# Kernel tuning notes

Hardware: AMD Instinct MI355X
Metric: run time of the kernel (lower is better)

The kernel has to match this reference:

```python
import jax, jax.numpy as jnp
import numpy as np
import math
from itertools import combinations

SEQ_LEN = 8
SET_SIZE = 3
IN_DIM = 2048
OUT_DIM = 1152
WAY = 5
SHOT = 5
N_QUERIES = 200
PE_SCALE = 0.1
LN_EPS = 1e-5
NEG_INF = -1e30

TUPLES = np.array(list(combinations(range(SEQ_LEN), SET_SIZE)), dtype=np.int32)  # [56, 3]
TUPLES_LEN = TUPLES.shape[0]


def _positional_encoding(d_model, max_len):
    position = np.arange(max_len)[:, None].astype(np.float32)
    div_term = np.exp(np.arange(0, d_model, 2).astype(np.float32) * -(math.log(10000.0) / d_model))
    pe = np.zeros((max_len, d_model), dtype=np.float32)
    pe[:, 0::2] = np.sin(position * div_term) * PE_SCALE
    pe[:, 1::2] = np.cos(position * div_term) * PE_SCALE
    return jnp.asarray(pe)

PE = _positional_encoding(IN_DIM, int(SEQ_LEN * 1.5))


def setup_inputs() -> dict:
    key = jax.random.key(0)
    ks = jax.random.split(key, 6)
    support_set = jax.random.normal(ks[0], (WAY * SHOT, SEQ_LEN, IN_DIM), dtype=jnp.float32)
    queries = jax.random.normal(ks[1], (N_QUERIES, SEQ_LEN, IN_DIM), dtype=jnp.float32)
    support_labels = jnp.repeat(jnp.arange(WAY, dtype=jnp.int32), SHOT)  # [25]
    Wk = jax.random.normal(ks[2], (IN_DIM * SET_SIZE, OUT_DIM), dtype=jnp.float32) * 0.02
    bk = jnp.zeros((OUT_DIM,), dtype=jnp.float32)
    Wv = jax.random.normal(ks[3], (IN_DIM * SET_SIZE, OUT_DIM), dtype=jnp.float32) * 0.02
    bv = jnp.zeros((OUT_DIM,), dtype=jnp.float32)
    ln_g = jnp.ones((OUT_DIM,), dtype=jnp.float32)
    ln_b = jnp.zeros((OUT_DIM,), dtype=jnp.float32)
    return {"support_set": support_set, "support_labels": support_labels, "queries": queries,
            "Wk": Wk, "bk": bk, "Wv": Wv, "bv": bv, "ln_g": ln_g, "ln_b": ln_b}


def _layernorm(x, g, b):
    mu = jnp.mean(x, axis=-1, keepdims=True)
    var = jnp.var(x, axis=-1, keepdims=True)
    return (x - mu) * jax.lax.rsqrt(var + LN_EPS) * g + b


def _tuple_features(x):
    # x: [N, SEQ_LEN, IN_DIM]; add PE (dropout is identity at inference), gather frame tuples.
    n = x.shape[0]
    x = x + PE[None, :x.shape[1], :]
    return x[:, TUPLES, :].reshape(n, TUPLES_LEN, SET_SIZE * IN_DIM)  # [N, 56, 6144]


def reference(support_set, support_labels, queries, Wk, bk, Wv, bv, ln_g, ln_b):
    n_q = queries.shape[0]
    s_feat = _tuple_features(support_set)   # [S, T, 6144]
    q_feat = _tuple_features(queries)       # [Q, T, 6144]

    sk = _layernorm(s_feat @ Wk + bk, ln_g, ln_b)  # [S, T, D]
    qk = _layernorm(q_feat @ Wk + bk, ln_g, ln_b)  # [Q, T, D]
    sv = s_feat @ Wv + bv                           # [S, T, D]
    qv = q_feat @ Wv + bv                           # [Q, T, D]

    # scores between every query tuple and every support tuple
    scores = jnp.einsum('qtd,skd->qtsk', qk, sk) / math.sqrt(OUT_DIM)  # [Q, T, S, T]

    # per-class masked softmax over (support clips of class c) x (support tuples)
    class_mask = support_labels[None, :] == jnp.arange(WAY, dtype=support_labels.dtype)[:, None]  # [WAY, S]
    masked = scores[None] + jnp.where(class_mask[:, None, None, :, None], 0.0, NEG_INF)  # [WAY, Q, T, S, T]
    attn = jax.nn.softmax(masked.reshape(WAY, n_q, TUPLES_LEN, -1), axis=-1)
    attn = attn.reshape(WAY, n_q, TUPLES_LEN, -1, TUPLES_LEN)  # [WAY, Q, T, S, T]

    proto = jnp.einsum('cqtsk,skd->cqtd', attn, sv)  # [WAY, Q, T, D]
    diff = qv[None] - proto                           # [WAY, Q, T, D]
    dist = -jnp.sum(diff * diff, axis=(2, 3)) / TUPLES_LEN  # [WAY, Q]
    return dist.T  # logits [Q, WAY]
```

## Files before the change

kernel.cpp:

```cpp
#include <hip/hip_runtime.h>
#include <math.h>

#define SEQ_LEN 8
#define IN_DIM 2048
#define OUT_DIM 1152
#define NTUP 56
#define NSUP 25
#define NQ 200
#define WAY 5
#define SFRAMES 200
#define NFRAMES 1800
#define SROWS 1400
#define QROWS 11200
#define AT_STRIDE 1440
#define KC 288
#define ALD 296

typedef __attribute__((ext_vector_type(8))) short short8;
typedef __attribute__((ext_vector_type(4))) float f32x4;

__device__ __constant__ int TUP[NTUP][3] = {
{0,1,2},{0,1,3},{0,1,4},{0,1,5},{0,1,6},{0,1,7},
{0,2,3},{0,2,4},{0,2,5},{0,2,6},{0,2,7},
{0,3,4},{0,3,5},{0,3,6},{0,3,7},
{0,4,5},{0,4,6},{0,4,7},
{0,5,6},{0,5,7},
{0,6,7},
{1,2,3},{1,2,4},{1,2,5},{1,2,6},{1,2,7},
{1,3,4},{1,3,5},{1,3,6},{1,3,7},
{1,4,5},{1,4,6},{1,4,7},
{1,5,6},{1,5,7},
{1,6,7},
{2,3,4},{2,3,5},{2,3,6},{2,3,7},
{2,4,5},{2,4,6},{2,4,7},
{2,5,6},{2,5,7},
{2,6,7},
{3,4,5},{3,4,6},{3,4,7},
{3,5,6},{3,5,7},
{3,6,7},
{4,5,6},{4,5,7},
{4,6,7},
{5,6,7}};

__device__ __forceinline__ unsigned short f2bf(float x) {
  union { float f; unsigned int u; } v; v.f = x;
  unsigned int r = v.u + 0x7fffu + ((v.u >> 16) & 1u);
  return (unsigned short)(r >> 16);
}
__device__ __forceinline__ float bf2f(unsigned short s) {
  union { float f; unsigned int u; } v; v.u = ((unsigned int)s) << 16;
  return v.f;
}

__device__ __forceinline__ void gll16(const void* g, void* l) {
  __builtin_amdgcn_global_load_lds(
      (const __attribute__((address_space(1))) unsigned int*)g,
      (__attribute__((address_space(3))) unsigned int*)l, 16, 0, 0);
}

#define APB_OFF   0UL
#define WT_OFF    7372800UL
#define PB_OFF    35684352UL
#define QKB_OFF   60567552UL
#define SKB_OFF   86372352UL
#define QVB_OFF   89597952UL
#define SVB_OFF   115402752UL
#define G2_OFF    118628352UL
#define SCB_OFF   119457792UL
#define G1B_OFF   151713792UL
#define QNORM_OFF 183969792UL
#define RANK_OFF  184014592UL

__global__ __launch_bounds__(256) void k_pre(const float* __restrict__ S,
                                             const float* __restrict__ Q,
                                             const float* __restrict__ Wk,
                                             const float* __restrict__ Wv,
                                             const int* __restrict__ labels,
                                             unsigned short* __restrict__ APb,
                                             unsigned short* __restrict__ WT,
                                             int* __restrict__ rank,
                                             float* __restrict__ outz) {
  __shared__ float t[32][33];
  int b = blockIdx.x, tid = threadIdx.x;
  if (b < NFRAMES) {
    int frame = b;
    int e8 = tid * 8;
    int pos = frame & 7;
    const float c0 = -logf(10000.0f) / (float)IN_DIM;
    float pe[8];
#pragma unroll
    for (int p = 0; p < 4; ++p) {
      float dt = expf((float)(e8 + 2 * p) * c0);
      float arg = (float)pos * dt;
      pe[2 * p] = sinf(arg) * 0.1f;
      pe[2 * p + 1] = cosf(arg) * 0.1f;
    }
    const float* src = (frame < SFRAMES) ? (S + (size_t)frame * IN_DIM + e8)
                                         : (Q + (size_t)(frame - SFRAMES) * IN_DIM + e8);
    float4 x0 = ((const float4*)src)[0], x1 = ((const float4*)src)[1];
    short8 o;
    o[0] = (short)f2bf(x0.x + pe[0]); o[1] = (short)f2bf(x0.y + pe[1]);
    o[2] = (short)f2bf(x0.z + pe[2]); o[3] = (short)f2bf(x0.w + pe[3]);
    o[4] = (short)f2bf(x1.x + pe[4]); o[5] = (short)f2bf(x1.y + pe[5]);
    o[6] = (short)f2bf(x1.z + pe[6]); o[7] = (short)f2bf(x1.w + pe[7]);
    *(short8*)(APb + (size_t)frame * IN_DIM + e8) = o;
  } else if (b < NFRAMES + 13824) {
    int z = b - NFRAMES;
    int bz = z / (64 * 36); int rem = z % (64 * 36);
    int by = rem / 64, bx = rem % 64;
    int w = bz / 3, j = bz % 3;
    const float* W = w ? Wv : Wk;
    int k0 = bx * 32, d0 = by * 32;
    int tx = tid & 31, ty = tid >> 5;
#pragma unroll
    for (int i = 0; i < 4; ++i) {
      int k = k0 + ty + i * 8;
      t[ty + i * 8][tx] = W[(size_t)(j * IN_DIM + k) * OUT_DIM + d0 + tx];
    }
    __syncthreads();
    int colbase = w * 3456 + j * 1152 + d0;
#pragma unroll
    for (int i = 0; i < 4; ++i) {
      int d = ty + i * 8;
      WT[(size_t)(colbase + d) * IN_DIM + k0 + tx] = f2bf(t[tx][d]);
    }
  } else {
    for (int i = tid; i < NQ * WAY; i += 256) outz[i] = 0.f;
    if (tid == 0) {
      for (int s = 0; s < NSUP; ++s) {
        int r = 0;
        for (int s2 = 0; s2 < NSUP; ++s2)
          r += (labels[s2] < labels[s]) || (labels[s2] == labels[s] && s2 < s);
        rank[s] = r;
      }
    }
  }
}

__device__ __forceinline__ void mfma_core(const short* __restrict__ A, int lda, int maxA,
                                          const short* __restrict__ B, int ldb, int maxB,
                                          int K, short* lds, f32x4 (&acc)[4][4]) {
  int tid = threadIdx.x;
  int lane = tid & 63, wave = tid >> 6;
  int wm = wave & 1, wn = wave >> 1;
  int col = lane & 15, quad = lane >> 4;
  short* As = lds;
  short* Bs = lds + 4096;
  int s0 = tid, s1 = tid + 256;
  int r0 = s0 >> 2, r1 = s1 >> 2;
  int o0 = (s0 & 3) * 8, o1 = (s1 & 3) * 8;
  const short* a0p = A + (size_t)min(r0, maxA) * lda + o0;
  const short* a1p = A + (size_t)min(r1, maxA) * lda + o1;
  const short* b0p = B + (size_t)min(r0, maxB) * ldb + o0;
  const short* b1p = B + (size_t)min(r1, maxB) * ldb + o1;
  short* la0 = As + s0 * 8; short* la1 = As + s1 * 8;
  short* lb0 = Bs + s0 * 8; short* lb1 = Bs + s1 * 8;

  for (int k0 = 0; k0 < K; k0 += 32) {
    gll16(a0p + k0, la0);
    gll16(a1p + k0, la1);
    gll16(b0p + k0, lb0);
    gll16(b1p + k0, lb1);
    __syncthreads();
    short8 af[4], bf[4];
#pragma unroll
    for (int i = 0; i < 4; ++i)
      af[i] = *(const short8*)(As + (wm * 64 + i * 16 + col) * 32 + quad * 8);
#pragma unroll
    for (int j = 0; j < 4; ++j)
      bf[j] = *(const short8*)(Bs + (wn * 64 + j * 16 + col) * 32 + quad * 8);
#pragma unroll
    for (int i = 0; i < 4; ++i)
#pragma unroll
      for (int j = 0; j < 4; ++j)
        acc[i][j] = __builtin_amdgcn_mfma_f32_16x16x32_bf16(af[i], bf[j], acc[i][j], 0, 0, 0);
    __syncthreads();
  }
}

__global__ __launch_bounds__(256) void k_gemm1(const unsigned short* __restrict__ APb,
                                               const unsigned short* __restrict__ WT,
                                               unsigned short* __restrict__ Pb) {
  __shared__ short lds[8192];
  int row0 = blockIdx.y * 128, col0 = blockIdx.x * 128;
  f32x4 acc[4][4];
#pragma unroll
  for (int i = 0; i < 4; ++i)
#pragma unroll
    for (int j = 0; j < 4; ++j) acc[i][j] = (f32x4)(0.f);
  mfma_core((const short*)APb + (size_t)row0 * IN_DIM, IN_DIM, min(127, NFRAMES - 1 - row0),
            (const short*)WT + (size_t)col0 * IN_DIM, IN_DIM, 127,
            IN_DIM, lds, acc);
  int lane = threadIdx.x & 63, wave = threadIdx.x >> 6;
  int wm = wave & 1, wn = wave >> 1, col = lane & 15, quad = lane >> 4;
#pragma unroll
  for (int i = 0; i < 4; ++i)
#pragma unroll
    for (int r = 0; r < 4; ++r) {
      int gr = row0 + wm * 64 + i * 16 + quad * 4 + r;
      if (gr >= NFRAMES) continue;
#pragma unroll
      for (int j = 0; j < 4; ++j)
        Pb[(size_t)gr * 6912 + col0 + wn * 64 + j * 16 + col] = f2bf(acc[i][j][r]);
    }
}

__global__ __launch_bounds__(256) void k_combine(const unsigned short* __restrict__ Pb,
                                                 const float* __restrict__ bk,
                                                 const float* __restrict__ bv,
                                                 const float* __restrict__ g,
                                                 const float* __restrict__ bb,
                                                 const int* __restrict__ rank,
                                                 unsigned short* __restrict__ SKb,
                                                 unsigned short* __restrict__ QKb,
                                                 unsigned short* __restrict__ SVb,
                                                 unsigned short* __restrict__ QVb,
                                                 float* __restrict__ qnorm) {
  __shared__ short L[8 * 3456];
  int n = blockIdx.x, w = blockIdx.y;
  int tid = threadIdx.x;
  bool sup = n < NSUP;
  int fbase = sup ? n * SEQ_LEN : SFRAMES + (n - NSUP) * SEQ_LEN;
  for (int i = 0; i < 14; ++i) {
    int idx = tid + 256 * i;
    if (idx < 3456) {
      int fr = idx / 432, off = (idx - fr * 432) * 8;
      *(short8*)(L + fr * 3456 + off) =
          *(const short8*)(Pb + (size_t)(fbase + fr) * 6912 + w * 3456 + off);
    }
  }
  __syncthreads();
  int wave = tid >> 6, lane = tid & 63;
  const float* bias = w ? bv : bk;
  float2 bi[9], gg[9], bbv[9];
#pragma unroll
  for (int i = 0; i < 9; ++i) {
    int p = lane + 64 * i;
    bi[i] = *(const float2*)(bias + 2 * p);
    if (w == 0) {
      gg[i] = *(const float2*)(g + 2 * p);
      bbv[i] = *(const float2*)(bb + 2 * p);
    }
  }
  int obase = sup ? rank[n] * NTUP : (n - NSUP) * NTUP;
  const unsigned int* Lu = (const unsigned int*)L;
  for (int t = wave; t < NTUP; t += 4) {
    int b0 = (TUP[t][0] * 3456) >> 1;
    int b1 = (TUP[t][1] * 3456 + 1152) >> 1;
    int b2 = (TUP[t][2] * 3456 + 2304) >> 1;
    float va[18];
    float sum = 0.f, sq = 0.f;
#pragma unroll
    for (int i = 0; i < 9; ++i) {
      int p = lane + 64 * i;
      unsigned int u0 = Lu[b0 + p], u1 = Lu[b1 + p], u2 = Lu[b2 + p];
      float a = bf2f((unsigned short)u0) + bf2f((unsigned short)u1) +
                bf2f((unsigned short)u2) + bi[i].x;
      float b = bf2f((unsigned short)(u0 >> 16)) + bf2f((unsigned short)(u1 >> 16)) +
                bf2f((unsigned short)(u2 >> 16)) + bi[i].y;
      va[2 * i] = a; va[2 * i + 1] = b;
      sum += a + b;
      sq += a * a + b * b;
    }
#pragma unroll
    for (int o = 32; o; o >>= 1) {
      sum += __shfl_xor(sum, o);
      sq += __shfl_xor(sq, o);
    }
    int orow = obase + t;
    if (w == 0) {
      float mean = sum * (1.f / OUT_DIM);
      float var = sq * (1.f / OUT_DIM) - mean * mean;
      float inv = rsqrtf(var + 1e-5f);
      unsigned short* outp = (sup ? SKb : QKb) + (size_t)orow * OUT_DIM;
#pragma unroll
      for (int i = 0; i < 9; ++i) {
        int p = lane + 64 * i;
        unsigned int lo = f2bf((va[2 * i] - mean) * inv * gg[i].x + bbv[i].x);
        unsigned int hi = f2bf((va[2 * i + 1] - mean) * inv * gg[i].y + bbv[i].y);
        *(unsigned int*)(outp + 2 * p) = lo | (hi << 16);
      }
    } else {
      unsigned short* outp = (sup ? SVb : QVb) + (size_t)orow * OUT_DIM;
#pragma unroll
      for (int i = 0; i < 9; ++i) {
        int p = lane + 64 * i;
        unsigned int lo = f2bf(va[2 * i]);
        unsigned int hi = f2bf(va[2 * i + 1]);
        *(unsigned int*)(outp + 2 * p) = lo | (hi << 16);
      }
      if (!sup && lane == 0) qnorm[orow] = sq;
    }
  }
}

__global__ __launch_bounds__(256) void k_rowgemm(const unsigned short* __restrict__ QKb,
                                                 const unsigned short* __restrict__ SKb,
                                                 const unsigned short* __restrict__ QVb,
                                                 const unsigned short* __restrict__ SVb,
                                                 unsigned short* __restrict__ SCb,
                                                 unsigned short* __restrict__ G1b,
                                                 unsigned short* __restrict__ G2) {
  __shared__ short lds[8192];
  int L = blockIdx.x;
  f32x4 acc[4][4];
#pragma unroll
  for (int i = 0; i < 4; ++i)
#pragma unroll
    for (int j = 0; j < 4; ++j) acc[i][j] = (f32x4)(0.f);
  int lane = threadIdx.x & 63, wave = threadIdx.x >> 6;
  int wm = wave & 1, wn = wave >> 1, col = lane & 15, quad = lane >> 4;

  if (L < 1936) {
    int l = L, g1 = 0;
    if (l >= 968) { g1 = 1; l -= 968; }
    int rowSub = l & 7, t = l >> 3;
    int colIdx = t % 11, rowGroup = t / 11;
    int row0 = (rowGroup * 8 + rowSub) << 7;
    int col0 = colIdx << 7;
    const unsigned short* Am = g1 ? QVb : QKb;
    const unsigned short* Bm = g1 ? SVb : SKb;
    mfma_core((const short*)Am + (size_t)row0 * OUT_DIM, OUT_DIM, min(127, QROWS - 1 - row0),
              (const short*)Bm + (size_t)col0 * OUT_DIM, OUT_DIM, min(127, SROWS - 1 - col0),
              OUT_DIM, lds, acc);
    unsigned short* outp = g1 ? G1b : SCb;
    const float scl = g1 ? 1.0f : 0.029462782549439483f;
#pragma unroll
    for (int i = 0; i < 4; ++i)
#pragma unroll
      for (int r = 0; r < 4; ++r) {
        int gr = row0 + wm * 64 + i * 16 + quad * 4 + r;
        if (gr >= QROWS) continue;
#pragma unroll
        for (int j = 0; j < 4; ++j) {
          int gc = col0 + wn * 64 + j * 16 + col;
          if (gc < SROWS) {
            int c = gc / 280;
            outp[(size_t)gr * AT_STRIDE + gc + c * 8] = f2bf(acc[i][j][r] * scl);
          }
        }
      }
  } else {
    int l = L - 1936;
    int c = l / 9, rem = l % 9;
    int i0 = (rem / 3) << 7, j0 = (rem % 3) << 7;
    const short* base = (const short*)SVb + (size_t)c * 280 * OUT_DIM;
    mfma_core(base + (size_t)i0 * OUT_DIM, OUT_DIM, min(127, 279 - i0),
              base + (size_t)j0 * OUT_DIM, OUT_DIM, min(127, 279 - j0),
              OUT_DIM, lds, acc);
    unsigned short* g2c = G2 + (size_t)c * KC * KC;
#pragma unroll
    for (int i = 0; i < 4; ++i)
#pragma unroll
      for (int r = 0; r < 4; ++r) {
        int gi = i0 + wm * 64 + i * 16 + quad * 4 + r;
        if (gi >= KC) continue;
#pragma unroll
        for (int j = 0; j < 4; ++j) {
          int gj = j0 + wn * 64 + j * 16 + col;
          if (gj < KC) g2c[(size_t)gi * KC + gj] = f2bf(acc[i][j][r]);
        }
      }
  }
}

__global__ __launch_bounds__(256) void k_attn(const unsigned short* __restrict__ SCb,
                                              const unsigned short* __restrict__ G1b,
                                              const unsigned short* __restrict__ G2,
                                              const float* __restrict__ qnorm,
                                              float* __restrict__ out) {
  __shared__ short attn[64 * ALD];
  __shared__ short Bs[64 * KC];
  __shared__ float T2n[64];
  __shared__ float Sarr[64];
  __shared__ float rowsum[64];
  __shared__ float val[64];
  int r0 = blockIdx.x * 64, c = blockIdx.y;
  int tid = threadIdx.x;

  int lr = tid >> 2, h = tid & 3;
  const unsigned short* ps = SCb + (size_t)(r0 + lr) * AT_STRIDE + c * KC;
  const unsigned short* pg = G1b + (size_t)(r0 + lr) * AT_STRIDE + c * KC;
  short8 sv[9];
  float mx = -INFINITY;
#pragma unroll
  for (int i = 0; i < 9; ++i) {
    int v = h * 9 + i;
    if (v < 35) {
      sv[i] = *(const short8*)(ps + v * 8);
#pragma unroll
      for (int j = 0; j < 8; ++j) mx = fmaxf(mx, bf2f((unsigned short)sv[i][j]));
    }
  }
  mx = fmaxf(mx, __shfl_xor(mx, 1));
  mx = fmaxf(mx, __shfl_xor(mx, 2));
  float sum = 0.f, t2 = 0.f;
#pragma unroll
  for (int i = 0; i < 9; ++i) {
    int v = h * 9 + i;
    if (v < 35) {
      short8 gv8 = *(const short8*)(pg + v * 8);
      short8 e8;
#pragma unroll
      for (int j = 0; j < 8; ++j) {
        float e = __expf(bf2f((unsigned short)sv[i][j]) - mx);
        sum += e;
        t2 += e * bf2f((unsigned short)gv8[j]);
        e8[j] = (short)f2bf(e);
      }
      *(short8*)(attn + lr * ALD + v * 8) = e8;
    } else {
      *(short8*)(attn + lr * ALD + v * 8) = (short8)0;
    }
  }
  sum += __shfl_xor(sum, 1); sum += __shfl_xor(sum, 2);
  t2 += __shfl_xor(t2, 1); t2 += __shfl_xor(t2, 2);
  if (h == 0) { Sarr[lr] = sum; T2n[lr] = t2; }
  if (tid < 64) rowsum[tid] = 0.f;
  __syncthreads();

  int lane = tid & 63, wave = tid >> 6;
  int col = lane & 15, quad = lane >> 4;
  const short* G2c = (const short*)G2 + (size_t)c * KC * KC;
  float part[4][4] = {};
  for (int j0 = 0; j0 < KC; j0 += 64) {
    int ncols = min(64, KC - j0);
    int chunks = ncols * 36;
    for (int base = 0; base < chunks; base += 256) {
      int idx = base + tid;
      if (idx < chunks) {
        int n = idx / 36, kk = idx - n * 36;
        gll16(G2c + (size_t)(j0 + n) * KC + kk * 8, Bs + idx * 8);
      }
    }
    __syncthreads();
    if (wave * 16 < ncols) {
      f32x4 acc[4];
#pragma unroll
      for (int i = 0; i < 4; ++i) acc[i] = (f32x4)(0.f);
      for (int kq = 0; kq < 9; ++kq) {
        short8 bf = *(const short8*)(Bs + (wave * 16 + col) * KC + kq * 32 + quad * 8);
#pragma unroll
        for (int i = 0; i < 4; ++i) {
          short8 af = *(const short8*)(attn + (i * 16 + col) * ALD + kq * 32 + quad * 8);
          acc[i] = __builtin_amdgcn_mfma_f32_16x16x32_bf16(af, bf, acc[i], 0, 0, 0);
        }
      }
      int gcol = j0 + wave * 16 + col;
#pragma unroll
      for (int i = 0; i < 4; ++i)
#pragma unroll
        for (int r = 0; r < 4; ++r)
          part[i][r] += bf2f((unsigned short)attn[(i * 16 + quad * 4 + r) * ALD + gcol]) *
                        acc[i][r];
    }
    __syncthreads();
  }
#pragma unroll
  for (int i = 0; i < 4; ++i)
#pragma unroll
    for (int r = 0; r < 4; ++r) {
      float s = part[i][r];
      s += __shfl_xor(s, 1); s += __shfl_xor(s, 2);
      s += __shfl_xor(s, 4); s += __shfl_xor(s, 8);
      if (col == 0) atomicAdd(&rowsum[i * 16 + quad * 4 + r], s);
    }
  __syncthreads();

  if (tid < 64) {
    float S = Sarr[tid], invS = 1.f / S;
    val[tid] = qnorm[r0 + tid] - 2.f * T2n[tid] * invS + rowsum[tid] * invS * invS;
  }
  __syncthreads();
  if (tid < 3) {
    int q = r0 / NTUP + tid;
    int lo = max(q * NTUP, r0), hi = min(q * NTUP + NTUP, r0 + 64);
    if (lo < hi && q < NQ) {
      float s = 0.f;
      for (int r = lo; r < hi; ++r) s += val[r - r0];
      atomicAdd(&out[q * WAY + c], -s * (1.f / NTUP));
    }
  }
}

extern "C" void kernel_launch(void* const* d_in, const int* in_sizes, int n_in,
                              void* d_out, int out_size, void* d_ws, size_t ws_size,
                              hipStream_t stream) {
  const float* support = (const float*)d_in[0];
  const int* labels = (const int*)d_in[1];
  const float* queries = (const float*)d_in[2];
  const float* Wk = (const float*)d_in[3];
  const float* bk = (const float*)d_in[4];
  const float* Wv = (const float*)d_in[5];
  const float* bv = (const float*)d_in[6];
  const float* ln_g = (const float*)d_in[7];
  const float* ln_b = (const float*)d_in[8];
  float* out = (float*)d_out;
  char* w8 = (char*)d_ws;

  unsigned short* APb = (unsigned short*)(w8 + APB_OFF);
  unsigned short* WT = (unsigned short*)(w8 + WT_OFF);
  unsigned short* Pb = (unsigned short*)(w8 + PB_OFF);
  unsigned short* QKb = (unsigned short*)(w8 + QKB_OFF);
  unsigned short* SKb = (unsigned short*)(w8 + SKB_OFF);
  unsigned short* QVb = (unsigned short*)(w8 + QVB_OFF);
  unsigned short* SVb = (unsigned short*)(w8 + SVB_OFF);
  unsigned short* G2 = (unsigned short*)(w8 + G2_OFF);
  unsigned short* SCb = (unsigned short*)(w8 + SCB_OFF);
  unsigned short* G1b = (unsigned short*)(w8 + G1B_OFF);
  float* QNORM = (float*)(w8 + QNORM_OFF);
  int* RANK = (int*)(w8 + RANK_OFF);

  k_pre<<<dim3(NFRAMES + 13824 + 1), dim3(256), 0, stream>>>(support, queries, Wk, Wv,
                                                             labels, APb, WT, RANK, out);
  k_gemm1<<<dim3(54, 15), dim3(256), 0, stream>>>(APb, WT, Pb);
  k_combine<<<dim3(225, 2), dim3(256), 0, stream>>>(Pb, bk, bv, ln_g, ln_b, RANK,
                                                    SKb, QKb, SVb, QVb, QNORM);
  k_rowgemm<<<dim3(1981), dim3(256), 0, stream>>>(QKb, SKb, QVb, SVb, SCb, G1b, G2);
  k_attn<<<dim3(175, 5), dim3(256), 0, stream>>>(SCb, G1b, G2, QNORM, out);
}
```

Before: 387.9 us.

## Multi-buffer LDS in MFMA GEMM core with prefetch depth two

Replaces the single-buffered load/sync/compute loop in the shared bf16 MFMA core with a 4-slot LDS ring. Global-to-LDS loads are issued two k-tiles ahead, and an explicit vmcnt wait plus a raw s_barrier replace the two __syncthreads per iteration. The MFMA block is also wrapped in s_setprio. The goal is to hide global load latency behind the matrix math. In exchange, LDS per block grows fourfold to 64 KB, which may reduce how many blocks fit on each CU.

```diff
diff --git a/kernel.cpp b/kernel.cpp
--- a/kernel.cpp
+++ b/kernel.cpp
@@ -58,6 +58,14 @@
       (__attribute__((address_space(3))) unsigned int*)l, 16, 0, 0);
 }
 
+#define VMCNT(N) asm volatile("s_waitcnt vmcnt(" #N ")" ::: "memory")
+
+__device__ __forceinline__ void pbar() {
+  asm volatile("" ::: "memory");
+  __builtin_amdgcn_s_barrier();
+  asm volatile("" ::: "memory");
+}
+
 #define APB_OFF   0UL
 #define WT_OFF    7372800UL
 #define PB_OFF    35684352UL
@@ -144,8 +152,6 @@
   int lane = tid & 63, wave = tid >> 6;
   int wm = wave & 1, wn = wave >> 1;
   int col = lane & 15, quad = lane >> 4;
-  short* As = lds;
-  short* Bs = lds + 4096;
   int s0 = tid, s1 = tid + 256;
   int r0 = s0 >> 2, r1 = s1 >> 2;
   int o0 = (s0 & 3) * 8, o1 = (s1 & 3) * 8;
@@ -153,15 +159,27 @@
   const short* a1p = A + (size_t)min(r1, maxA) * lda + o1;
   const short* b0p = B + (size_t)min(r0, maxB) * ldb + o0;
   const short* b1p = B + (size_t)min(r1, maxB) * ldb + o1;
-  short* la0 = As + s0 * 8; short* la1 = As + s1 * 8;
-  short* lb0 = Bs + s0 * 8; short* lb1 = Bs + s1 * 8;
-
-  for (int k0 = 0; k0 < K; k0 += 32) {
-    gll16(a0p + k0, la0);
-    gll16(a1p + k0, la1);
-    gll16(b0p + k0, lb0);
-    gll16(b1p + k0, lb1);
-    __syncthreads();
+  const int nt = K >> 5;
+
+#define STAGE(t)                                     \
+  do {                                               \
+    short* buf_ = lds + (((t) & 3) << 13);           \
+    int k0_ = (t) << 5;                              \
+    gll16(a0p + k0_, buf_ + s0 * 8);                 \
+    gll16(a1p + k0_, buf_ + s1 * 8);                 \
+    gll16(b0p + k0_, buf_ + 4096 + s0 * 8);          \
+    gll16(b1p + k0_, buf_ + 4096 + s1 * 8);          \
+  } while (0)
+
+  STAGE(0);
+  STAGE(1);
+  VMCNT(4);
+  pbar();
+
+  for (int t = 0; t < nt; ++t) {
+    if (t + 2 < nt) STAGE(t + 2);
+    const short* As = lds + ((t & 3) << 13);
+    const short* Bs = As + 4096;
     short8 af[4], bf[4];
 #pragma unroll
     for (int i = 0; i < 4; ++i)
@@ -169,19 +187,24 @@
 #pragma unroll
     for (int j = 0; j < 4; ++j)
       bf[j] = *(const short8*)(Bs + (wn * 64 + j * 16 + col) * 32 + quad * 8);
+    __builtin_amdgcn_s_setprio(1);
 #pragma unroll
     for (int i = 0; i < 4; ++i)
 #pragma unroll
       for (int j = 0; j < 4; ++j)
         acc[i][j] = __builtin_amdgcn_mfma_f32_16x16x32_bf16(af[i], bf[j], acc[i][j], 0, 0, 0);
-    __syncthreads();
-  }
+    __builtin_amdgcn_s_setprio(0);
+    if (t + 2 < nt) VMCNT(4);
+    else            VMCNT(0);
+    pbar();
+  }
+#undef STAGE
 }
 
 __global__ __launch_bounds__(256) void k_gemm1(const unsigned short* __restrict__ APb,
                                                const unsigned short* __restrict__ WT,
                                                unsigned short* __restrict__ Pb) {
-  __shared__ short lds[8192];
+  __shared__ short lds[32768];
   int row0 = blockIdx.y * 128, col0 = blockIdx.x * 128;
   f32x4 acc[4][4];
 #pragma unroll
@@ -301,7 +324,7 @@
                                                  unsigned short* __restrict__ SCb,
                                                  unsigned short* __restrict__ G1b,
                                                  unsigned short* __restrict__ G2) {
-  __shared__ short lds[8192];
+  __shared__ short lds[32768];
   int L = blockIdx.x;
   f32x4 acc[4][4];
 #pragma unroll
```

New measurement: 370.3 us. 1.05x faster.
